# Kernel tuning notes

Measured on AMD Instinct MI355X. Metric: run time of the kernel, lower is better.

The kernel has to match this reference:

```python
import jax, jax.numpy as jnp
import numpy as np

EPS = 1e-8
TEMP3 = 10.0


def setup_inputs() -> dict:
    key = jax.random.key(0)
    k1, k2, k3 = jax.random.split(key, 3)
    B, D = 8192, 512
    cnn_code = jax.random.normal(k1, (B, D), dtype=jnp.float32)
    rnn_code = jax.random.normal(k2, (B, D), dtype=jnp.float32)
    idx = jax.random.uniform(k3, (B, B), dtype=jnp.float32)
    # ensure every row has at least one positive (> threshold1=0.8), as the
    # original divides by len(pos)
    diag = jnp.arange(B)
    idx = idx.at[diag, diag].set(0.95)
    probs = jnp.array([0.8, 0.5], dtype=jnp.float32)  # (threshold1, threshold2)
    return {"cnn_code": cnn_code, "rnn_code": rnn_code, "idx": idx, "probs": probs}


def reference(cnn_code, rnn_code, idx, probs):
    B = cnn_code.shape[0]
    fdt = cnn_code.dtype
    # cosine similarity * temp3  -> scores0 [B,B]
    cn = jnp.linalg.norm(cnn_code, axis=-1, keepdims=True)   # [B,1]
    rn = jnp.linalg.norm(rnn_code, axis=-1, keepdims=True)   # [B,1]
    scores0 = (cnn_code @ rnn_code.T) / jnp.clip(cn * rn.T, EPS) * TEMP3
    scores1 = scores0.T

    th1, th2 = probs[0], probs[1]
    pos_mask = idx > th1    # [B,B] ragged positive sets per row
    neg_mask = idx <= th2   # [B,B] ragged negative sets per row
    n_pos = pos_mask.sum(axis=1).astype(fdt)          # [B]
    n_neg = neg_mask.sum(axis=1).astype(fdt)          # [B]

    neginf = jnp.array(-jnp.inf, dtype=fdt)
    # logsumexp over each row's negative set (shared across all positives j)
    lse_neg0 = jax.nn.logsumexp(jnp.where(neg_mask, scores0, neginf), axis=1)  # [B]
    lse_neg1 = jax.nn.logsumexp(jnp.where(neg_mask, scores1, neginf), axis=1)  # [B]

    # For each positive j: logits = concat([score_j, neg_scores]); target puts
    # mass 1 on index 0; softXEnt divides by logits length (1 + n_neg).
    denom = (1.0 + n_neg)[:, None]                                            # [B,1]
    l0 = -(scores0 - jnp.logaddexp(scores0, lse_neg0[:, None])) / denom       # [B,B]
    l1 = -(scores1 - jnp.logaddexp(scores1, lse_neg1[:, None])) / denom

    loss0 = (jnp.where(pos_mask, l0, 0.0).sum(axis=1) / n_pos).sum() / B
    loss1 = (jnp.where(pos_mask, l1, 0.0).sum(axis=1) / n_pos).sum() / B
    return loss0 + loss1
```

## Files before the change

kernel.cpp:

```cpp
#include <hip/hip_runtime.h>
#include <hip/hip_bf16.h>
#include <math.h>
#include <stdint.h>

#define BDIM 8192
#define DDIM 512
#define NT   64
#define BK   64
#define TEMP 10.0f

typedef __attribute__((ext_vector_type(8))) short bf16x8;
typedef __attribute__((ext_vector_type(4))) float f32x4;
typedef unsigned long long u64;
typedef unsigned int u32;

__device__ __forceinline__ unsigned short f2bf(float f) {
  unsigned int x = __float_as_uint(f);
  x += 0x7fffu + ((x >> 16) & 1u);
  return (unsigned short)(x >> 16);
}

__device__ __forceinline__ void gld16(const void* gptr, void* lptr) {
  __builtin_amdgcn_global_load_lds((const __attribute__((address_space(1))) u32*)gptr,
                                   (__attribute__((address_space(3))) u32*)lptr, 16, 0, 0);
}

__device__ __forceinline__ float red16_dpp(float x) {
  x += __int_as_float(__builtin_amdgcn_mov_dpp(__float_as_int(x), 0xB1, 0xF, 0xF, true));
  x += __int_as_float(__builtin_amdgcn_mov_dpp(__float_as_int(x), 0x4E, 0xF, 0xF, true));
  x += __int_as_float(__builtin_amdgcn_mov_dpp(__float_as_int(x), 0x141, 0xF, 0xF, true));
  x += __int_as_float(__builtin_amdgcn_mov_dpp(__float_as_int(x), 0x140, 0xF, 0xF, true));
  return x;
}

__global__ __launch_bounds__(256) void knorm(const float* __restrict__ cnn,
                                             const float* __restrict__ rnn,
                                             unsigned short* __restrict__ u,
                                             unsigned short* __restrict__ v) {
  int wid = threadIdx.x >> 6, lane = threadIdx.x & 63;
  int gw = blockIdx.x * 4 + wid;
  const float* src;
  unsigned short* dst;
  int row;
  float mul;
  if (gw < BDIM) { src = cnn; dst = u; row = gw; mul = TEMP; }
  else           { src = rnn; dst = v; row = gw - BDIM; mul = 1.0f; }
  const float* p = src + (size_t)row * DDIM + lane * 8;
  float4 a0 = *(const float4*)p;
  float4 a1 = *(const float4*)(p + 4);
  float ss = a0.x*a0.x + a0.y*a0.y + a0.z*a0.z + a0.w*a0.w
           + a1.x*a1.x + a1.y*a1.y + a1.z*a1.z + a1.w*a1.w;
#pragma unroll
  for (int m = 1; m <= 32; m <<= 1) ss += __shfl_xor(ss, m);
  float inv = mul / sqrtf(ss);
  unsigned short o[8];
  o[0] = f2bf(a0.x * inv); o[1] = f2bf(a0.y * inv);
  o[2] = f2bf(a0.z * inv); o[3] = f2bf(a0.w * inv);
  o[4] = f2bf(a1.x * inv); o[5] = f2bf(a1.y * inv);
  o[6] = f2bf(a1.z * inv); o[7] = f2bf(a1.w * inv);
  *(uint4*)(dst + (size_t)row * DDIM + lane * 8) = *(uint4*)o;
}

__global__ __launch_bounds__(256, 3) void kmain(const unsigned short* __restrict__ u,
                                                const unsigned short* __restrict__ v,
                                                const float* __restrict__ idx,
                                                const float* __restrict__ probs,
                                                float* __restrict__ P) {
  __shared__ unsigned short aT[128 * BK];
  __shared__ unsigned short bT[128 * BK];
  __shared__ float L0[5 * 128];
  __shared__ float L1[3 * 128];
  __shared__ u64 m0p[128][2], m0n[128][2];
  __shared__ u64 m1p[128][2], m1n[128][2];
  const int tid = threadIdx.x, lane = tid & 63, wid = tid >> 6;
  const int l15 = lane & 15, lg = lane >> 4;
  const int qr = wid >> 1, qc = wid & 1;

  for (int t = tid; t < 1024; t += 256) {
    if (t < 640) L0[t] = 0.f; else L1[t - 640] = 0.f;
  }

  const int bid = blockIdx.x;
  const int xcd = bid & 7, n = bid >> 3;
  const int st = n >> 6, w = n & 63;
  const int ti = xcd * 8 + (w & 7);
  const int tj = st * 8 + (w >> 3);
  const int I = ti * 128, J = tj * 128;

  const float th1 = probs[0], th2 = probs[1];
#pragma unroll 1
  for (int b = 0; b < 8; ++b) {
    float x[8];
#pragma unroll
    for (int t = 0; t < 8; ++t) {
      int i = b * 8 + t;
      int r = wid * 32 + (i >> 1), h = i & 1;
      x[t] = idx[(size_t)(I + r) * BDIM + J + h * 64 + lane];
    }
#pragma unroll
    for (int t = 0; t < 8; ++t) {
      int i = b * 8 + t;
      int r = wid * 32 + (i >> 1), h = i & 1;
      u64 pb = __ballot(x[t] > th1);
      u64 nb = __ballot(x[t] <= th2);
      if (lane == 0) { m0p[r][h] = pb; m0n[r][h] = nb; }
    }
  }
#pragma unroll 1
  for (int b = 0; b < 8; ++b) {
    float x[8];
#pragma unroll
    for (int t = 0; t < 8; ++t) {
      int i = b * 8 + t;
      int r = wid * 32 + (i >> 1), h = i & 1;
      x[t] = idx[(size_t)(J + r) * BDIM + I + h * 64 + lane];
    }
#pragma unroll
    for (int t = 0; t < 8; ++t) {
      int i = b * 8 + t;
      int r = wid * 32 + (i >> 1), h = i & 1;
      u64 pb = __ballot(x[t] > th1);
      u64 nb = __ballot(x[t] <= th2);
      if (lane == 0) { m1p[r][h] = pb; m1n[r][h] = nb; }
    }
  }

  f32x4 acc[4][4];
#pragma unroll
  for (int a = 0; a < 4; a++)
#pragma unroll
    for (int b = 0; b < 4; b++) acc[a][b] = (f32x4){0, 0, 0, 0};

  const unsigned short* gA = u + (size_t)(I + wid * 32 + (lane >> 3)) * DDIM + (lane & 7) * 8;
  const unsigned short* gB = v + (size_t)(J + wid * 32 + (lane >> 3)) * DDIM + (lane & 7) * 8;
  unsigned short* lA = aT + (wid * 32 + (lane >> 3)) * BK + (lane & 7) * 8;
  unsigned short* lB = bT + (wid * 32 + (lane >> 3)) * BK + (lane & 7) * 8;

  for (int k0 = 0; k0 < DDIM; k0 += BK) {
#pragma unroll
    for (int c = 0; c < 4; c++) {
      gld16(gA + (size_t)c * 8 * DDIM + k0, lA + c * 8 * BK);
      gld16(gB + (size_t)c * 8 * DDIM + k0, lB + c * 8 * BK);
    }
    __syncthreads();
#pragma unroll
    for (int kk = 0; kk < 2; kk++) {
      bf16x8 af[4], bf_[4];
#pragma unroll
      for (int ar = 0; ar < 4; ar++)
        af[ar] = *(const bf16x8*)(aT + (qr * 64 + ar * 16 + l15) * BK + kk * 32 + lg * 8);
#pragma unroll
      for (int bc = 0; bc < 4; bc++)
        bf_[bc] = *(const bf16x8*)(bT + (qc * 64 + bc * 16 + l15) * BK + kk * 32 + lg * 8);
#pragma unroll
      for (int ar = 0; ar < 4; ar++)
#pragma unroll
        for (int bc = 0; bc < 4; bc++)
          acc[ar][bc] = __builtin_amdgcn_mfma_f32_16x16x32_bf16(af[ar], bf_[bc], acc[ar][bc], 0, 0, 0);
    }
    __syncthreads();
  }

  u64 pw1[4], nw1[4];
#pragma unroll
  for (int bc = 0; bc < 4; bc++) {
    int C = qc * 64 + bc * 16 + l15;
    pw1[bc] = m1p[C][qr] >> (lg * 4);
    nw1[bc] = m1n[C][qr] >> (lg * 4);
  }

  float zn1[4] = {0, 0, 0, 0}, zp1[4] = {0, 0, 0, 0}, sm1[4] = {0, 0, 0, 0};

#pragma unroll
  for (int ar = 0; ar < 4; ar++) {
    u64 pw[4], nw[4];
#pragma unroll
    for (int j = 0; j < 4; j++) {
      int R = qr * 64 + ar * 16 + lg * 4 + j;
      pw[j] = m0p[R][qc] >> l15;
      nw[j] = m0n[R][qc] >> l15;
    }
#pragma unroll
    for (int j = 0; j < 4; j++) {
      float zn0 = 0, zp0 = 0, sm0 = 0, cp0 = 0, cn0 = 0;
#pragma unroll
      for (int bc = 0; bc < 4; bc++) {
        float s = acc[ar][bc][j];
        float e = __expf(s - TEMP);
        float mp0 = (float)((unsigned)(pw[j]  >> (bc * 16)) & 1u);
        float mn0 = (float)((unsigned)(nw[j]  >> (bc * 16)) & 1u);
        float mp1 = (float)((unsigned)(pw1[bc] >> (ar * 16 + j)) & 1u);
        float mn1 = (float)((unsigned)(nw1[bc] >> (ar * 16 + j)) & 1u);
        zp0 = fmaf(mp0, e, zp0);
        sm0 = fmaf(mp0, s, sm0);
        zn0 = fmaf(mn0, e, zn0);
        cp0 += mp0;
        cn0 += mn0;
        zp1[bc] = fmaf(mp1, e, zp1[bc]);
        sm1[bc] = fmaf(mp1, s, sm1[bc]);
        zn1[bc] = fmaf(mn1, e, zn1[bc]);
      }
      zn0 = red16_dpp(zn0); zp0 = red16_dpp(zp0); sm0 = red16_dpp(sm0);
      cp0 = red16_dpp(cp0); cn0 = red16_dpp(cn0);
      if (l15 == 0) {
        int R = qr * 64 + ar * 16 + lg * 4 + j;
        atomicAdd(&L0[0 * 128 + R], zn0);
        atomicAdd(&L0[1 * 128 + R], zp0);
        atomicAdd(&L0[2 * 128 + R], sm0);
        atomicAdd(&L0[3 * 128 + R], cp0);
        atomicAdd(&L0[4 * 128 + R], cn0);
      }
    }
  }

#pragma unroll
  for (int bc = 0; bc < 4; bc++) {
    float zn = zn1[bc], zp = zp1[bc], sm = sm1[bc];
    zn += __shfl_xor(zn, 16); zn += __shfl_xor(zn, 32);
    zp += __shfl_xor(zp, 16); zp += __shfl_xor(zp, 32);
    sm += __shfl_xor(sm, 16); sm += __shfl_xor(sm, 32);
    if (lg == 0) {
      int C = qc * 64 + bc * 16 + l15;
      atomicAdd(&L1[0 * 128 + C], zn);
      atomicAdd(&L1[1 * 128 + C], zp);
      atomicAdd(&L1[2 * 128 + C], sm);
    }
  }
  __syncthreads();

  for (int t = tid; t < 1024; t += 256) {
    int s = t >> 7, c = t & 127;
    if (s < 5) P[((size_t)tj * 8 + s) * BDIM + I + c] = L0[s * 128 + c];
    else       P[((size_t)ti * 8 + s) * BDIM + J + c] = L1[(s - 5) * 128 + c];
  }
}

__global__ __launch_bounds__(128) void kfinal(const float* __restrict__ P,
                                              float* __restrict__ part) {
  int r = blockIdx.x * 128 + threadIdx.x;
  float st[8] = {0, 0, 0, 0, 0, 0, 0, 0};
  for (int k = 0; k < 64; k++) {
#pragma unroll
    for (int s = 0; s < 8; s++) st[s] += P[((size_t)k * 8 + s) * BDIM + r];
  }
  float np = st[3], nn = st[4];
  float inv = 1.f / (np * (1.f + nn));
  float l0 = (np * (TEMP + logf(st[0])) - st[2] + st[1] / st[0]) * inv;
  float l1 = (np * (TEMP + logf(st[5])) - st[7] + st[6] / st[5]) * inv;
  float tot = l0 + l1;
#pragma unroll
  for (int m = 1; m <= 32; m <<= 1) tot += __shfl_xor(tot, m);
  __shared__ float sb;
  if (threadIdx.x == 0) sb = tot;
  __syncthreads();
  if (threadIdx.x == 64) part[blockIdx.x] = sb + tot;
}

__global__ __launch_bounds__(64) void kfinal2(const float* __restrict__ part,
                                              float* __restrict__ out) {
  float t = part[threadIdx.x];
#pragma unroll
  for (int m = 1; m <= 32; m <<= 1) t += __shfl_xor(t, m);
  if (threadIdx.x == 0) out[0] = t / (float)BDIM;
}

extern "C" void kernel_launch(void* const* d_in, const int* in_sizes, int n_in,
                              void* d_out, int out_size, void* d_ws, size_t ws_size,
                              hipStream_t stream) {
  (void)in_sizes; (void)n_in; (void)out_size; (void)ws_size;
  const float* cnn   = (const float*)d_in[0];
  const float* rnn   = (const float*)d_in[1];
  const float* idx   = (const float*)d_in[2];
  const float* probs = (const float*)d_in[3];
  char* w = (char*)d_ws;
  unsigned short* u  = (unsigned short*)w;
  unsigned short* v  = (unsigned short*)(w + 8388608);
  float* P    = (float*)(w + 16777216);
  float* part = (float*)(w + 33554432);

  knorm<<<(2 * BDIM) / 4, 256, 0, stream>>>(cnn, rnn, u, v);
  kmain<<<NT * NT, 256, 0, stream>>>(u, v, idx, probs, P);
  kfinal<<<BDIM / 128, 128, 0, stream>>>(P, part);
  kfinal2<<<1, 64, 0, stream>>>(part, (float*)d_out);
}
```

Measured before the change: 258.4 us.

## Interleave idx mask loading with GEMM k-loop and XOR-swizzle LDS tiles

The idx mask reads and ballots, which used to run as a separate prologue, now happen inside the GEMM k-loop. Each iteration loads four rows of both idx tiles alongside the async global-to-LDS loads, so the idx traffic overlaps with the MFMA work. The LDS tile layout is also XOR-swizzled, with the swizzle applied on the global source address and on the fragment reads, to cut LDS bank conflicts. In exchange, register pressure inside the loop goes up.

```diff
diff --git a/kernel.cpp b/kernel.cpp
--- a/kernel.cpp
+++ b/kernel.cpp
@@ -88,42 +88,6 @@
   const int I = ti * 128, J = tj * 128;
 
   const float th1 = probs[0], th2 = probs[1];
-#pragma unroll 1
-  for (int b = 0; b < 8; ++b) {
-    float x[8];
-#pragma unroll
-    for (int t = 0; t < 8; ++t) {
-      int i = b * 8 + t;
-      int r = wid * 32 + (i >> 1), h = i & 1;
-      x[t] = idx[(size_t)(I + r) * BDIM + J + h * 64 + lane];
-    }
-#pragma unroll
-    for (int t = 0; t < 8; ++t) {
-      int i = b * 8 + t;
-      int r = wid * 32 + (i >> 1), h = i & 1;
-      u64 pb = __ballot(x[t] > th1);
-      u64 nb = __ballot(x[t] <= th2);
-      if (lane == 0) { m0p[r][h] = pb; m0n[r][h] = nb; }
-    }
-  }
-#pragma unroll 1
-  for (int b = 0; b < 8; ++b) {
-    float x[8];
-#pragma unroll
-    for (int t = 0; t < 8; ++t) {
-      int i = b * 8 + t;
-      int r = wid * 32 + (i >> 1), h = i & 1;
-      x[t] = idx[(size_t)(J + r) * BDIM + I + h * 64 + lane];
-    }
-#pragma unroll
-    for (int t = 0; t < 8; ++t) {
-      int i = b * 8 + t;
-      int r = wid * 32 + (i >> 1), h = i & 1;
-      u64 pb = __ballot(x[t] > th1);
-      u64 nb = __ballot(x[t] <= th2);
-      if (lane == 0) { m1p[r][h] = pb; m1n[r][h] = nb; }
-    }
-  }
 
   f32x4 acc[4][4];
 #pragma unroll
@@ -131,27 +95,52 @@
 #pragma unroll
     for (int b = 0; b < 4; b++) acc[a][b] = (f32x4){0, 0, 0, 0};
 
-  const unsigned short* gA = u + (size_t)(I + wid * 32 + (lane >> 3)) * DDIM + (lane & 7) * 8;
-  const unsigned short* gB = v + (size_t)(J + wid * 32 + (lane >> 3)) * DDIM + (lane & 7) * 8;
+  const int srcsw = ((lane & 7) ^ ((lane >> 3) & 7)) * 8;
+  const unsigned short* gA = u + (size_t)(I + wid * 32 + (lane >> 3)) * DDIM + srcsw;
+  const unsigned short* gB = v + (size_t)(J + wid * 32 + (lane >> 3)) * DDIM + srcsw;
   unsigned short* lA = aT + (wid * 32 + (lane >> 3)) * BK + (lane & 7) * 8;
   unsigned short* lB = bT + (wid * 32 + (lane >> 3)) * BK + (lane & 7) * 8;
-
-  for (int k0 = 0; k0 < DDIM; k0 += BK) {
+  const int rsw = (l15 & 7);
+
+  for (int t = 0; t < 8; ++t) {
+    const int k0 = t * BK;
 #pragma unroll
     for (int c = 0; c < 4; c++) {
       gld16(gA + (size_t)c * 8 * DDIM + k0, lA + c * 8 * BK);
       gld16(gB + (size_t)c * 8 * DDIM + k0, lB + c * 8 * BK);
     }
+    const int rbase = wid * 32 + t * 4;
+    float mx0[4][2], mx1[4][2];
+#pragma unroll
+    for (int rr = 0; rr < 4; rr++)
+#pragma unroll
+      for (int h = 0; h < 2; h++) {
+        mx0[rr][h] = idx[(size_t)(I + rbase + rr) * BDIM + J + h * 64 + lane];
+        mx1[rr][h] = idx[(size_t)(J + rbase + rr) * BDIM + I + h * 64 + lane];
+      }
     __syncthreads();
+#pragma unroll
+    for (int rr = 0; rr < 4; rr++)
+#pragma unroll
+      for (int h = 0; h < 2; h++) {
+        u64 p0 = __ballot(mx0[rr][h] > th1);
+        u64 n0 = __ballot(mx0[rr][h] <= th2);
+        u64 p1 = __ballot(mx1[rr][h] > th1);
+        u64 n1 = __ballot(mx1[rr][h] <= th2);
+        if (lane == 0) {
+          m0p[rbase + rr][h] = p0; m0n[rbase + rr][h] = n0;
+          m1p[rbase + rr][h] = p1; m1n[rbase + rr][h] = n1;
+        }
+      }
 #pragma unroll
     for (int kk = 0; kk < 2; kk++) {
       bf16x8 af[4], bf_[4];
 #pragma unroll
       for (int ar = 0; ar < 4; ar++)
-        af[ar] = *(const bf16x8*)(aT + (qr * 64 + ar * 16 + l15) * BK + kk * 32 + lg * 8);
+        af[ar] = *(const bf16x8*)(aT + (qr * 64 + ar * 16 + l15) * BK + ((kk * 4 + lg) ^ rsw) * 8);
 #pragma unroll
       for (int bc = 0; bc < 4; bc++)
-        bf_[bc] = *(const bf16x8*)(bT + (qc * 64 + bc * 16 + l15) * BK + kk * 32 + lg * 8);
+        bf_[bc] = *(const bf16x8*)(bT + (qc * 64 + bc * 16 + l15) * BK + ((kk * 4 + lg) ^ rsw) * 8);
 #pragma unroll
       for (int ar = 0; ar < 4; ar++)
 #pragma unroll
```

New measurement: 212.5 us. -17.8%, faster.
